# Kernel optimization log

Hardware: AMD Instinct MI355X
Metric: run time of the kernel (lower is better)

Reference implementation:

```python
import jax, jax.numpy as jnp
import numpy as np

N = 100000   # nodes
E = 1250000  # edges per graph
D = 64       # in_feats
H = 64       # hidden_dim
C = 129      # num_classes
EPS = 1e-5


def setup_inputs() -> dict:
    key = jax.random.key(0)
    ks = jax.random.split(key, 32)
    nrm = lambda k, s: jax.random.normal(k, s, jnp.float32) * 0.05
    inp = {
        'node_features': jax.random.normal(ks[0], (N, D), jnp.float32),
        'm_src': jax.random.randint(ks[1], (E,), 0, N, jnp.int32),
        'm_dst': jax.random.randint(ks[2], (E,), 0, N, jnp.int32),
        'r_src': jax.random.randint(ks[3], (E,), 0, N, jnp.int32),
        'r_dst': jax.random.randint(ks[4], (E,), 0, N, jnp.int32),
    }
    i = 5
    for pre in ('soc', 'rt'):
        inp[pre + '_W1'] = nrm(ks[i], (D, H)); inp[pre + '_b1'] = jnp.zeros((H,), jnp.float32)
        inp[pre + '_g1'] = jnp.ones((H,), jnp.float32); inp[pre + '_bt1'] = jnp.zeros((H,), jnp.float32)
        inp[pre + '_W2'] = nrm(ks[i + 1], (H, H)); inp[pre + '_b2'] = jnp.zeros((H,), jnp.float32)
        inp[pre + '_g2'] = jnp.ones((H,), jnp.float32); inp[pre + '_bt2'] = jnp.zeros((H,), jnp.float32)
        i += 2
    inp['gW1'] = nrm(ks[i], (4 * H, H)); inp['gb1'] = jnp.zeros((H,), jnp.float32)
    inp['prelu_a'] = jnp.full((1,), 0.25, jnp.float32)
    inp['gW2'] = nrm(ks[i + 1], (H, H)); inp['gb2'] = jnp.zeros((H,), jnp.float32)
    inp['fcW'] = nrm(ks[i + 2], (H, C)); inp['fcb'] = jnp.zeros((C,), jnp.float32)
    return inp


def _gconv(h, src, dst, W, b):
    # DGL GraphConv, norm='both': D_out^{-1/2} (scatter-sum) D_in^{-1/2}, linear, ELU
    ones = jnp.ones(src.shape[0], jnp.float32)
    deg_o = jax.ops.segment_sum(ones, src, num_segments=N)
    deg_i = jax.ops.segment_sum(ones, dst, num_segments=N)
    ns = jax.lax.rsqrt(jnp.clip(deg_o, 1.0))
    nd = jax.lax.rsqrt(jnp.clip(deg_i, 1.0))
    agg = jax.ops.segment_sum((h * ns[:, None])[src], dst, num_segments=N)
    return jax.nn.elu((agg * nd[:, None]) @ W + b)


def _bn(x, g, b):
    mu = x.mean(0)
    v = x.var(0)
    return (x - mu) * jax.lax.rsqrt(v + EPS) * g + b


def _branch(x, src, dst, W1, b1, g1, bt1, W2, b2, g2, bt2):
    h = _bn(_gconv(x, src, dst, W1, b1), g1, bt1)
    return _bn(_gconv(h, src, dst, W2, b2), g2, bt2)


def reference(node_features, m_src, m_dst, r_src, r_dst,
              soc_W1, soc_b1, soc_g1, soc_bt1, soc_W2, soc_b2, soc_g2, soc_bt2,
              rt_W1, rt_b1, rt_g1, rt_bt1, rt_W2, rt_b2, rt_g2, rt_bt2,
              gW1, gb1, prelu_a, gW2, gb2, fcW, fcb):
    h1 = _branch(node_features, m_src, m_dst, soc_W1, soc_b1, soc_g1, soc_bt1, soc_W2, soc_b2, soc_g2, soc_bt2)
    h2 = _branch(node_features, r_src, r_dst, rt_W1, rt_b1, rt_g1, rt_bt1, rt_W2, rt_b2, rt_g2, rt_bt2)
    cat = jnp.concatenate([h1, h2, jnp.abs(h1 - h2), h1 * h2], axis=-1)
    z = cat @ gW1 + gb1
    z = jnp.where(z > 0, z, prelu_a * z)  # PReLU (single shared slope)
    gate = jax.nn.sigmoid(z @ gW2 + gb2)
    fused = gate * h1 + (1.0 - gate) * h2
    return fused @ fcW + fcb
```

## Files before the change

kernel.cpp:

```cpp
#include <hip/hip_runtime.h>
#include <math.h>

#define NN 100000
#define NE 1250000
#define HD 64
#define NCLS 129
#define NTILES 6250
#define GRID_T 782
#define MAXDEG 64

#define NCH 64
#define CHU ((NE + NCH - 1) / NCH)
#define SUBR 50000
#define NW2 12500
#define NHE2 ((NN + 1) * (size_t)HD)

typedef float f32x4 __attribute__((ext_vector_type(4)));
typedef short bf16x8 __attribute__((ext_vector_type(8)));

__device__ __forceinline__ short f2b(float f) {
    unsigned u = __builtin_bit_cast(unsigned, f);
    u += 0x7FFFu + ((u >> 16) & 1u);
    return (short)(u >> 16);
}
__device__ __forceinline__ float b2f(short s) {
    return __builtin_bit_cast(float, ((unsigned)(unsigned short)s) << 16);
}

__global__ __launch_bounds__(1024) void k_hist8(
    const int* __restrict__ d0, const int* __restrict__ s0,
    const int* __restrict__ d1, const int* __restrict__ s1,
    unsigned char* __restrict__ P8d, unsigned char* __restrict__ P8s) {
    __shared__ unsigned int hw[NW2];
    int b = blockIdx.x, s = blockIdx.y, z = blockIdx.z;
    int g = z >> 1, arr = z & 1;
    const int* __restrict__ idx = arr ? (g ? s1 : s0) : (g ? d1 : d0);
    for (int i = threadIdx.x; i < NW2; i += 1024) hw[i] = 0;
    __syncthreads();
    int lo = s * SUBR;
    int beg = b * CHU, end = beg + CHU;
    if (end > NE) end = NE;
    for (int i = beg + threadIdx.x; i < end; i += 1024) {
        int v = idx[i] - lo;
        if ((unsigned)v < (unsigned)SUBR)
            atomicAdd(&hw[v >> 2], 1u << ((v & 3) * 8));
    }
    __syncthreads();
    unsigned char* base = arr ? P8s : P8d;
    unsigned int* dst = (unsigned int*)(base + ((size_t)(g * NCH + b)) * NN + lo);
    for (int i = threadIdx.x; i < NW2; i += 1024) dst[i] = hw[i];
}

__global__ void k_reduce8(unsigned int* __restrict__ Pd, const unsigned int* __restrict__ Ps,
                          float* __restrict__ ns, float* __restrict__ nd,
                          int* __restrict__ degi) {
    int w = blockIdx.x * 256 + threadIdx.x;
    if (w >= NN / 4) return;
    int g = blockIdx.y;
    Pd += (size_t)g * NCH * (NN / 4);
    Ps += (size_t)g * NCH * (NN / 4);
    ns += (size_t)g * (NN + 1); nd += (size_t)g * NN; degi += (size_t)g * NN;
    if (w == 0) ns[NN] = 0.f;
    unsigned run = 0;
#pragma unroll 8
    for (int b = 0; b < NCH; ++b) {
        size_t o = (size_t)b * (NN / 4) + w;
        unsigned v = Pd[o];
        Pd[o] = run;
        run += v;
    }
    unsigned so = 0;
#pragma unroll 8
    for (int b = 0; b < NCH; ++b) so += Ps[(size_t)b * (NN / 4) + w];
#pragma unroll
    for (int j = 0; j < 4; ++j) {
        int din = (run >> (8 * j)) & 255;
        int dout = (so >> (8 * j)) & 255;
        int node = w * 4 + j;
        degi[node] = din;
        ns[node] = rsqrtf((float)(dout < 1 ? 1 : dout));
        nd[node] = rsqrtf((float)(din < 1 ? 1 : din));
    }
}

__global__ __launch_bounds__(1024) void k_fill8(
    const int* __restrict__ d0, const int* __restrict__ d1,
    const int* __restrict__ s0, const int* __restrict__ s1,
    const unsigned char* __restrict__ Pofs, int* __restrict__ col) {
    __shared__ unsigned int cur[NW2];
    int b = blockIdx.x, s = blockIdx.y, g = blockIdx.z;
    const int* __restrict__ dst = g ? d1 : d0;
    const int* __restrict__ src = g ? s1 : s0;
    col += ((size_t)g * NN) * MAXDEG;
    const unsigned char* __restrict__ ofs = Pofs + ((size_t)(g * NCH + b)) * NN;
    for (int i = threadIdx.x; i < NW2; i += 1024) cur[i] = 0;
    __syncthreads();
    int lo = s * SUBR;
    int beg = b * CHU, end = beg + CHU;
    if (end > NE) end = NE;
    for (int i = beg + threadIdx.x; i < end; i += 1024) {
        int d = dst[i] - lo;
        if ((unsigned)d < (unsigned)SUBR) {
            unsigned old = atomicAdd(&cur[d >> 2], 1u << ((d & 3) * 8));
            int r = (old >> ((d & 3) * 8)) & 255;
            int node = d + lo;
            col[(size_t)node * MAXDEG + (int)ofs[node] + r] = src[i];
        }
    }
}

__global__ void k_scale_nf(const float* __restrict__ nf, short* __restrict__ T) {
    int i = blockIdx.x * blockDim.x + threadIdx.x;
    if (i >= (NN + 1) * 8) return;
    int node = i >> 3;
    short r[8];
    if (node == NN) {
#pragma unroll
        for (int j = 0; j < 8; ++j) r[j] = 0;
    } else {
        const float4* p = (const float4*)(nf + (size_t)i * 8);
        float4 a = p[0], b = p[1];
        r[0] = f2b(a.x); r[1] = f2b(a.y); r[2] = f2b(a.z); r[3] = f2b(a.w);
        r[4] = f2b(b.x); r[5] = f2b(b.y); r[6] = f2b(b.z); r[7] = f2b(b.w);
    }
    *(bf16x8*)(T + (size_t)i * 8) = *(bf16x8*)r;
}

template <int BN>
__global__ __launch_bounds__(256) void k_gather(
    const short* __restrict__ tab, size_t tabStride,
    const float* __restrict__ ns, const float* __restrict__ nd,
    const int* __restrict__ degi, const int* __restrict__ col,
    short* __restrict__ out, const float* __restrict__ stats,
    const float* __restrict__ ga, const float* __restrict__ gb,
    const float* __restrict__ bta, const float* __restrict__ btb) {
    int w = (blockIdx.x * 256 + threadIdx.x) >> 6;
    int lane = threadIdx.x & 63;
    if (w >= NN) return;
    int g = blockIdx.y;
    tab += (size_t)g * tabStride; nd += (size_t)g * NN; degi += (size_t)g * NN;
    col += ((size_t)g * NN) * MAXDEG; out += (size_t)g * NHE2;
    const float* nsA = ns + (size_t)g * (NN + 1);
    int grp = lane >> 4;
    int sub = lane & 15;
    int deg = degi[w];
    int myc = (lane < deg) ? col[(size_t)w * MAXDEG + lane] : NN;
    float myns = nsA[myc];
    float a0 = 0.f, a1 = 0.f, a2 = 0.f, a3 = 0.f, sl = 0.f;
    for (int j = 0; j < deg; j += 16) {
#pragma unroll
        for (int u = 0; u < 4; ++u) {
            int idx = j + u * 4 + grp;
            int c = __shfl(myc, idx, 64);
            float nsc = __shfl(myns, idx, 64);
            uint2 v = *(const uint2*)(tab + (size_t)c * HD + sub * 4);
            a0 = fmaf(nsc, __builtin_bit_cast(float, v.x << 16), a0);
            a1 = fmaf(nsc, __builtin_bit_cast(float, v.x & 0xffff0000u), a1);
            a2 = fmaf(nsc, __builtin_bit_cast(float, v.y << 16), a2);
            a3 = fmaf(nsc, __builtin_bit_cast(float, v.y & 0xffff0000u), a3);
            if (BN) sl += nsc;
        }
    }
    a0 += __shfl_xor(a0, 16, 64); a1 += __shfl_xor(a1, 16, 64);
    a2 += __shfl_xor(a2, 16, 64); a3 += __shfl_xor(a3, 16, 64);
    a0 += __shfl_xor(a0, 32, 64); a1 += __shfl_xor(a1, 32, 64);
    a2 += __shfl_xor(a2, 32, 64); a3 += __shfl_xor(a3, 32, 64);
    if (BN) { sl += __shfl_xor(sl, 16, 64); sl += __shfl_xor(sl, 32, 64); }
    if (grp == 0) {
        float s = nd[w];
        float r4[4] = {a0, a1, a2, a3};
        if (BN) {
            const float* gp = g ? gb : ga;
            const float* bp = g ? btb : bta;
            const float* st = stats + (size_t)g * 128;
            const float invN = 1.f / (float)NN;
#pragma unroll
            for (int q = 0; q < 4; ++q) {
                int o = sub * 4 + q;
                float mu = st[o] * invN;
                float var = fmaxf(st[64 + o] * invN - mu * mu, 0.f);
                float isd = rsqrtf(var + 1e-5f);
                float sc = gp[o] * isd;
                float sh = bp[o] - mu * sc;
                r4[q] = s * (sc * r4[q] + sh * sl);
            }
        } else {
#pragma unroll
            for (int q = 0; q < 4; ++q) r4[q] *= s;
        }
        unsigned r0 = ((unsigned)(unsigned short)f2b(r4[0])) |
                      (((unsigned)(unsigned short)f2b(r4[1])) << 16);
        unsigned r1 = ((unsigned)(unsigned short)f2b(r4[2])) |
                      (((unsigned)(unsigned short)f2b(r4[3])) << 16);
        uint2 r; r.x = r0; r.y = r1;
        *(uint2*)(out + (size_t)w * HD + sub * 4) = r;
    }
}

__global__ __launch_bounds__(256) void k_lin(
    const short* __restrict__ X, const float* __restrict__ Wa, const float* __restrict__ Wb,
    const float* __restrict__ ba, const float* __restrict__ bb,
    short* __restrict__ Y, float* __restrict__ stats) {
    __shared__ short sW[4096];
    __shared__ float sm2[128];
    int g = blockIdx.y;
    const float* W = g ? Wb : Wa;
    const float* bias = g ? bb : ba;
    X += (size_t)g * NHE2; Y += (size_t)g * NHE2; stats += (size_t)g * 128;
    int t = threadIdx.x;
    for (int i = t; i < 4096; i += 256) {
        int j = i & 7, l16i = (i >> 3) & 15, kgi = (i >> 7) & 3, kbi = (i >> 9) & 1, oti = (i >> 10) & 3;
        sW[i] = f2b(W[(kbi * 32 + kgi * 8 + j) * HD + oti * 16 + l16i]);
    }
    if (t < 128) sm2[t] = 0.f;
    __syncthreads();
    int lane = t & 63, wv = t >> 6, l16 = lane & 15, kg = lane >> 4;
    bf16x8 bfrag[2][4];
#pragma unroll
    for (int kb = 0; kb < 2; ++kb)
#pragma unroll
        for (int ot = 0; ot < 4; ++ot)
            bfrag[kb][ot] = *(const bf16x8*)&sW[((ot * 2 + kb) * 4 + kg) * 128 + l16 * 8];
    float bo[4];
#pragma unroll
    for (int ot = 0; ot < 4; ++ot) bo[ot] = bias[ot * 16 + l16];
    float ps[4] = {0.f, 0.f, 0.f, 0.f}, pq[4] = {0.f, 0.f, 0.f, 0.f};
    for (int tile = blockIdx.x * 4 + wv; tile < NTILES; tile += GRID_T * 4) {
        const short* xp = X + ((size_t)tile * 16 + l16) * HD + kg * 8;
        bf16x8 a0 = *(const bf16x8*)xp;
        bf16x8 a1 = *(const bf16x8*)(xp + 32);
        f32x4 acc[4];
#pragma unroll
        for (int ot = 0; ot < 4; ++ot) {
            acc[ot] = (f32x4){0.f, 0.f, 0.f, 0.f};
            acc[ot] = __builtin_amdgcn_mfma_f32_16x16x32_bf16(a0, bfrag[0][ot], acc[ot], 0, 0, 0);
            acc[ot] = __builtin_amdgcn_mfma_f32_16x16x32_bf16(a1, bfrag[1][ot], acc[ot], 0, 0, 0);
        }
#pragma unroll
        for (int ot = 0; ot < 4; ++ot) {
#pragma unroll
            for (int r = 0; r < 4; ++r) {
                float y = acc[ot][r] + bo[ot];
                y = y > 0.f ? y : expm1f(y);
                ps[ot] += y; pq[ot] += y * y;
                Y[((size_t)tile * 16 + kg * 4 + r) * HD + ot * 16 + l16] = f2b(y);
            }
        }
    }
#pragma unroll
    for (int ot = 0; ot < 4; ++ot) {
        atomicAdd(&sm2[ot * 16 + l16], ps[ot]);
        atomicAdd(&sm2[64 + ot * 16 + l16], pq[ot]);
    }
    __syncthreads();
    if (t < 128) atomicAdd(&stats[t], sm2[t]);
}

__global__ void k_bnb(const short* __restrict__ Y, short* __restrict__ O,
                      const float* __restrict__ stats,
                      const float* __restrict__ ga, const float* __restrict__ gb,
                      const float* __restrict__ bta, const float* __restrict__ btb) {
    int i = blockIdx.x * blockDim.x + threadIdx.x;
    if (i >= NN * 8) return;
    int gI = blockIdx.y;
    Y += (size_t)gI * NHE2; O += (size_t)gI * NHE2; stats += (size_t)gI * 128;
    const float* g = gI ? gb : ga;
    const float* bt = gI ? btb : bta;
    int o0 = (i & 7) * 8;
    bf16x8 v = *(const bf16x8*)(Y + (size_t)i * 8);
    short r[8];
    const float invN = 1.f / (float)NN;
#pragma unroll
    for (int j = 0; j < 8; ++j) {
        int o = o0 + j;
        float mu = stats[o] * invN;
        float var = fmaxf(stats[64 + o] * invN - mu * mu, 0.f);
        float isd = rsqrtf(var + 1e-5f);
        float sc = g[o] * isd;
        float sh = bt[o] - mu * sc;
        r[j] = f2b(b2f(v[j]) * sc + sh);
    }
    *(bf16x8*)(O + (size_t)i * 8) = *(bf16x8*)r;
}

#define TRS 72
__global__ __launch_bounds__(256) void k_tail(
    const short* __restrict__ H1, const short* __restrict__ H2,
    const float* __restrict__ W1, const float* __restrict__ bias1,
    const float* __restrict__ pa,
    const float* __restrict__ W2, const float* __restrict__ bias2,
    const float* __restrict__ Wf, const float* __restrict__ biasf,
    float* __restrict__ out) {
    __shared__ short sW1[16384];
    __shared__ short sW2[4096];
    __shared__ short sWf[9216];
    __shared__ short tr[4][2][16 * TRS];
    int t = threadIdx.x;
    for (int i = t; i < 16384; i += 256) {
        int j = i & 7, l16i = (i >> 3) & 15, kgi = (i >> 7) & 3, kbi = (i >> 9) & 7, oti = (i >> 12) & 3;
        sW1[i] = f2b(W1[(kbi * 32 + kgi * 8 + j) * HD + oti * 16 + l16i]);
    }
    for (int i = t; i < 4096; i += 256) {
        int j = i & 7, l16i = (i >> 3) & 15, kgi = (i >> 7) & 3, kbi = (i >> 9) & 1, oti = (i >> 10) & 3;
        sW2[i] = f2b(W2[(kbi * 32 + kgi * 8 + j) * HD + oti * 16 + l16i]);
    }
    for (int i = t; i < 9216; i += 256) {
        int j = i & 7, l16i = (i >> 3) & 15, kgi = (i >> 7) & 3, kbi = (i >> 9) & 1, oti = i >> 10;
        int k = kbi * 32 + kgi * 8 + j, o = oti * 16 + l16i;
        sWf[i] = (o < NCLS) ? f2b(Wf[k * NCLS + o]) : (short)0;
    }
    __syncthreads();
    int lane = t & 63, wv = t >> 6, l16 = lane & 15, kg = lane >> 4;
    float slope = pa[0];
    float bo1[4], bo2[4], bof[9];
#pragma unroll
    for (int ot = 0; ot < 4; ++ot) { bo1[ot] = bias1[ot * 16 + l16]; bo2[ot] = bias2[ot * 16 + l16]; }
#pragma unroll
    for (int ot = 0; ot < 9; ++ot) {
        int o = ot * 16 + l16;
        bof[ot] = (o < NCLS) ? biasf[o] : 0.f;
    }
    bf16x8 b2frag[2][4];
#pragma unroll
    for (int kb = 0; kb < 2; ++kb)
#pragma unroll
        for (int ot = 0; ot < 4; ++ot)
            b2frag[kb][ot] = *(const bf16x8*)&sW2[((ot * 2 + kb) * 4 + kg) * 128 + l16 * 8];
    short* trZ = &tr[wv][0][0];
    short* trG = &tr[wv][1][0];

    for (int tile = blockIdx.x * 4 + wv; tile < NTILES; tile += GRID_T * 4) {
        size_t rb = ((size_t)tile * 16 + l16) * HD + kg * 8;
        bf16x8 h1e = *(const bf16x8*)(H1 + rb);
        bf16x8 h1o = *(const bf16x8*)(H1 + rb + 32);
        bf16x8 h2e = *(const bf16x8*)(H2 + rb);
        bf16x8 h2o = *(const bf16x8*)(H2 + rb + 32);
        bf16x8 fe[8];
        fe[0] = h1e; fe[1] = h1o; fe[2] = h2e; fe[3] = h2o;
        short tabs[8], tprd[8];
#pragma unroll
        for (int j = 0; j < 8; ++j) {
            float a = b2f(h1e[j]), b = b2f(h2e[j]);
            tabs[j] = f2b(fabsf(a - b)); tprd[j] = f2b(a * b);
        }
        fe[4] = *(bf16x8*)tabs; fe[6] = *(bf16x8*)tprd;
#pragma unroll
        for (int j = 0; j < 8; ++j) {
            float a = b2f(h1o[j]), b = b2f(h2o[j]);
            tabs[j] = f2b(fabsf(a - b)); tprd[j] = f2b(a * b);
        }
        fe[5] = *(bf16x8*)tabs; fe[7] = *(bf16x8*)tprd;
        f32x4 acc[4];
#pragma unroll
        for (int ot = 0; ot < 4; ++ot) acc[ot] = (f32x4){0.f, 0.f, 0.f, 0.f};
#pragma unroll
        for (int kb = 0; kb < 8; ++kb)
#pragma unroll
            for (int ot = 0; ot < 4; ++ot) {
                bf16x8 bf = *(const bf16x8*)&sW1[((ot * 8 + kb) * 4 + kg) * 128 + l16 * 8];
                acc[ot] = __builtin_amdgcn_mfma_f32_16x16x32_bf16(fe[kb], bf, acc[ot], 0, 0, 0);
            }
#pragma unroll
        for (int ot = 0; ot < 4; ++ot)
#pragma unroll
            for (int r = 0; r < 4; ++r) {
                float z = acc[ot][r] + bo1[ot];
                z = z > 0.f ? z : slope * z;
                trZ[(kg * 4 + r) * TRS + ot * 16 + l16] = f2b(z);
            }
        asm volatile("s_waitcnt lgkmcnt(0)" ::: "memory");
        __builtin_amdgcn_sched_barrier(0);
        bf16x8 za0 = *(const bf16x8*)&trZ[l16 * TRS + kg * 8];
        bf16x8 za1 = *(const bf16x8*)&trZ[l16 * TRS + 32 + kg * 8];
        f32x4 acc2[4];
#pragma unroll
        for (int ot = 0; ot < 4; ++ot) {
            acc2[ot] = (f32x4){0.f, 0.f, 0.f, 0.f};
            acc2[ot] = __builtin_amdgcn_mfma_f32_16x16x32_bf16(za0, b2frag[0][ot], acc2[ot], 0, 0, 0);
            acc2[ot] = __builtin_amdgcn_mfma_f32_16x16x32_bf16(za1, b2frag[1][ot], acc2[ot], 0, 0, 0);
        }
#pragma unroll
        for (int ot = 0; ot < 4; ++ot)
#pragma unroll
            for (int r = 0; r < 4; ++r) {
                float y = acc2[ot][r] + bo2[ot];
                float gate = 1.f / (1.f + expf(-y));
                trG[(kg * 4 + r) * TRS + ot * 16 + l16] = f2b(gate);
            }
        asm volatile("s_waitcnt lgkmcnt(0)" ::: "memory");
        __builtin_amdgcn_sched_barrier(0);
        bf16x8 ga0 = *(const bf16x8*)&trG[l16 * TRS + kg * 8];
        bf16x8 ga1 = *(const bf16x8*)&trG[l16 * TRS + 32 + kg * 8];
        short f0[8], f1[8];
#pragma unroll
        for (int j = 0; j < 8; ++j) {
            float gf = b2f(ga0[j]);
            f0[j] = f2b(gf * b2f(h1e[j]) + (1.f - gf) * b2f(h2e[j]));
            float gf2 = b2f(ga1[j]);
            f1[j] = f2b(gf2 * b2f(h1o[j]) + (1.f - gf2) * b2f(h2o[j]));
        }
        bf16x8 fa0 = *(bf16x8*)f0, fa1 = *(bf16x8*)f1;
        f32x4 acc3[9];
#pragma unroll
        for (int ot = 0; ot < 9; ++ot) acc3[ot] = (f32x4){0.f, 0.f, 0.f, 0.f};
#pragma unroll
        for (int kb = 0; kb < 2; ++kb) {
            bf16x8 a = kb ? fa1 : fa0;
#pragma unroll
            for (int ot = 0; ot < 9; ++ot) {
                bf16x8 bf = *(const bf16x8*)&sWf[((ot * 2 + kb) * 4 + kg) * 128 + l16 * 8];
                acc3[ot] = __builtin_amdgcn_mfma_f32_16x16x32_bf16(a, bf, acc3[ot], 0, 0, 0);
            }
        }
#pragma unroll
        for (int ot = 0; ot < 9; ++ot) {
            int o = ot * 16 + l16;
            if (o < NCLS) {
#pragma unroll
                for (int r = 0; r < 4; ++r) {
                    int node = tile * 16 + kg * 4 + r;
                    out[(size_t)node * NCLS + o] = acc3[ot][r] + bof[ot];
                }
            }
        }
    }
}

extern "C" void kernel_launch(void* const* d_in, const int* in_sizes, int n_in,
                              void* d_out, int out_size, void* d_ws, size_t ws_size,
                              hipStream_t stream) {
    (void)in_sizes; (void)n_in; (void)out_size; (void)ws_size;
    const int N = NN;

    const float* nf = (const float*)d_in[0];
    const int* m_src = (const int*)d_in[1];
    const int* m_dst = (const int*)d_in[2];
    const int* r_src = (const int*)d_in[3];
    const int* r_dst = (const int*)d_in[4];
    const float *W1[2], *b1[2], *g1[2], *bt1[2], *W2[2], *b2[2], *g2[2], *bt2[2];
    for (int br = 0; br < 2; ++br) {
        int base = 5 + br * 8;
        W1[br] = (const float*)d_in[base + 0];
        b1[br] = (const float*)d_in[base + 1];
        g1[br] = (const float*)d_in[base + 2];
        bt1[br] = (const float*)d_in[base + 3];
        W2[br] = (const float*)d_in[base + 4];
        b2[br] = (const float*)d_in[base + 5];
        g2[br] = (const float*)d_in[base + 6];
        bt2[br] = (const float*)d_in[base + 7];
    }
    const float* gW1 = (const float*)d_in[21];
    const float* gb1 = (const float*)d_in[22];
    const float* pa  = (const float*)d_in[23];
    const float* gW2 = (const float*)d_in[24];
    const float* gb2 = (const float*)d_in[25];
    const float* fcW = (const float*)d_in[26];
    const float* fcb = (const float*)d_in[27];
    float* out = (float*)d_out;

    char* p = (char*)d_ws;
    auto take = [&](size_t bytes) { char* r = p; p += (bytes + 255) & ~(size_t)255; return r; };
    size_t NHb2 = NHE2 * 2;
    unsigned char* P8d = (unsigned char*)take((size_t)2 * NCH * NN);
    unsigned char* P8s = (unsigned char*)take((size_t)2 * NCH * NN);
    int* col  = (int*)take((size_t)2 * NN * MAXDEG * 4);
    short* T  = (short*)take(NHb2);
    short* X  = (short*)take(2 * NHb2);
    short* Y  = (short*)take(2 * NHb2);
    short* H  = (short*)take(2 * NHb2);
    float* ns = (float*)take((size_t)2 * (N + 1) * 4);
    float* nd = (float*)take((size_t)2 * N * 4);
    float* stats = (float*)take(2 * 2 * 128 * 4);
    int* degi = (int*)take((size_t)2 * N * 4);

    int gEWz = ((N + 1) * 8 + 255) / 256;
    int gEW  = (N * 8 + 255) / 256;
    int gW4 = (N / 4 + 255) / 256;
    int gGat = (N * 64) / 256;

    k_hist8<<<dim3(NCH, 2, 4), 1024, 0, stream>>>(m_dst, m_src, r_dst, r_src, P8d, P8s);
    k_reduce8<<<dim3(gW4, 2), 256, 0, stream>>>((unsigned int*)P8d, (const unsigned int*)P8s,
                                                ns, nd, degi);
    k_fill8<<<dim3(NCH, 2, 2), 1024, 0, stream>>>(m_dst, r_dst, m_src, r_src, P8d, col);
    hipMemsetAsync(stats, 0, 2 * 2 * 128 * 4, stream);

    k_scale_nf<<<gEWz, 256, 0, stream>>>(nf, T);
    k_gather<0><<<dim3(gGat, 2), 256, 0, stream>>>(T, 0, ns, nd, degi, col, X,
                                                   nullptr, nullptr, nullptr, nullptr, nullptr);
    k_lin<<<dim3(GRID_T, 2), 256, 0, stream>>>(X, W1[0], W1[1], b1[0], b1[1], Y, stats);

    k_gather<1><<<dim3(gGat, 2), 256, 0, stream>>>(Y, NHE2, ns, nd, degi, col, X,
                                                   stats, g1[0], g1[1], bt1[0], bt1[1]);
    k_lin<<<dim3(GRID_T, 2), 256, 0, stream>>>(X, W2[0], W2[1], b2[0], b2[1], Y, stats + 256);
    k_bnb<<<dim3(gEW, 2), 256, 0, stream>>>(Y, H, stats + 256, g2[0], g2[1], bt2[0], bt2[1]);

    k_tail<<<GRID_T, 256, 0, stream>>>(H, H + NHE2, gW1, gb1, pa, gW2, gb2, fcW, fcb, out);
}
```

Measured before the change: 370.8 us.

## Prescale layer-1 output by source norm and widen gather loads to 16 bytes

The first linear kernel now multiplies its ELU output by the source-degree norm before storing it. The second gather therefore becomes a plain sum without a per-edge shuffle or FMA by ns. The per-node sum of ns, needed to fold in the BN shift, is computed once in the first gather and stored for reuse. The gather also switches from 8-byte to 16-byte row loads, with 8 lanes per row and 8 edges in flight, which cuts the number of shuffle-reduction steps. The cost is an extra buffer, an ns read per row in k_lin, and zeroing the dummy row.

```diff
diff --git a/kernel.cpp b/kernel.cpp
--- a/kernel.cpp
+++ b/kernel.cpp
@@ -126,12 +126,13 @@
     *(bf16x8*)(T + (size_t)i * 8) = *(bf16x8*)r;
 }
 
-template <int BN>
+template <int PHASE>
 __global__ __launch_bounds__(256) void k_gather(
     const short* __restrict__ tab, size_t tabStride,
     const float* __restrict__ ns, const float* __restrict__ nd,
     const int* __restrict__ degi, const int* __restrict__ col,
-    short* __restrict__ out, const float* __restrict__ stats,
+    short* __restrict__ out, float* __restrict__ sns,
+    const float* __restrict__ stats,
     const float* __restrict__ ga, const float* __restrict__ gb,
     const float* __restrict__ bta, const float* __restrict__ btb) {
     int w = (blockIdx.x * 256 + threadIdx.x) >> 6;
@@ -139,74 +140,92 @@
     if (w >= NN) return;
     int g = blockIdx.y;
     tab += (size_t)g * tabStride; nd += (size_t)g * NN; degi += (size_t)g * NN;
-    col += ((size_t)g * NN) * MAXDEG; out += (size_t)g * NHE2;
+    col += ((size_t)g * NN) * MAXDEG; out += (size_t)g * NHE2; sns += (size_t)g * NN;
     const float* nsA = ns + (size_t)g * (NN + 1);
-    int grp = lane >> 4;
-    int sub = lane & 15;
+    int grp = lane >> 3;
+    int sub = lane & 7;
     int deg = degi[w];
     int myc = (lane < deg) ? col[(size_t)w * MAXDEG + lane] : NN;
-    float myns = nsA[myc];
-    float a0 = 0.f, a1 = 0.f, a2 = 0.f, a3 = 0.f, sl = 0.f;
-    for (int j = 0; j < deg; j += 16) {
+    float myns = 0.f;
+    if (PHASE == 0) myns = nsA[myc];
+    float a[8] = {0.f, 0.f, 0.f, 0.f, 0.f, 0.f, 0.f, 0.f};
+    float sl = 0.f;
+    for (int j = 0; j < deg; j += 32) {
 #pragma unroll
         for (int u = 0; u < 4; ++u) {
-            int idx = j + u * 4 + grp;
+            int idx = j + u * 8 + grp;
             int c = __shfl(myc, idx, 64);
-            float nsc = __shfl(myns, idx, 64);
-            uint2 v = *(const uint2*)(tab + (size_t)c * HD + sub * 4);
-            a0 = fmaf(nsc, __builtin_bit_cast(float, v.x << 16), a0);
-            a1 = fmaf(nsc, __builtin_bit_cast(float, v.x & 0xffff0000u), a1);
-            a2 = fmaf(nsc, __builtin_bit_cast(float, v.y << 16), a2);
-            a3 = fmaf(nsc, __builtin_bit_cast(float, v.y & 0xffff0000u), a3);
-            if (BN) sl += nsc;
-        }
-    }
-    a0 += __shfl_xor(a0, 16, 64); a1 += __shfl_xor(a1, 16, 64);
-    a2 += __shfl_xor(a2, 16, 64); a3 += __shfl_xor(a3, 16, 64);
-    a0 += __shfl_xor(a0, 32, 64); a1 += __shfl_xor(a1, 32, 64);
-    a2 += __shfl_xor(a2, 32, 64); a3 += __shfl_xor(a3, 32, 64);
-    if (BN) { sl += __shfl_xor(sl, 16, 64); sl += __shfl_xor(sl, 32, 64); }
+            uint4 v = *(const uint4*)(tab + (size_t)c * HD + sub * 8);
+            unsigned wd[4] = {v.x, v.y, v.z, v.w};
+            if (PHASE == 0) {
+                float nsc = __shfl(myns, idx, 64);
+                sl += nsc;
+#pragma unroll
+                for (int q = 0; q < 4; ++q) {
+                    a[2 * q]     = fmaf(nsc, __builtin_bit_cast(float, wd[q] << 16), a[2 * q]);
+                    a[2 * q + 1] = fmaf(nsc, __builtin_bit_cast(float, wd[q] & 0xffff0000u), a[2 * q + 1]);
+                }
+            } else {
+#pragma unroll
+                for (int q = 0; q < 4; ++q) {
+                    a[2 * q]     += __builtin_bit_cast(float, wd[q] << 16);
+                    a[2 * q + 1] += __builtin_bit_cast(float, wd[q] & 0xffff0000u);
+                }
+            }
+        }
+    }
+#pragma unroll
+    for (int m = 8; m <= 32; m <<= 1) {
+#pragma unroll
+        for (int q = 0; q < 8; ++q) a[q] += __shfl_xor(a[q], m, 64);
+        if (PHASE == 0) sl += __shfl_xor(sl, m, 64);
+    }
     if (grp == 0) {
         float s = nd[w];
-        float r4[4] = {a0, a1, a2, a3};
-        if (BN) {
+        float r8[8];
+        if (PHASE == 1) {
             const float* gp = g ? gb : ga;
             const float* bp = g ? btb : bta;
             const float* st = stats + (size_t)g * 128;
+            float slv = sns[w];
             const float invN = 1.f / (float)NN;
 #pragma unroll
-            for (int q = 0; q < 4; ++q) {
-                int o = sub * 4 + q;
+            for (int q = 0; q < 8; ++q) {
+                int o = sub * 8 + q;
                 float mu = st[o] * invN;
                 float var = fmaxf(st[64 + o] * invN - mu * mu, 0.f);
                 float isd = rsqrtf(var + 1e-5f);
                 float sc = gp[o] * isd;
                 float sh = bp[o] - mu * sc;
-                r4[q] = s * (sc * r4[q] + sh * sl);
+                r8[q] = s * (sc * a[q] + sh * slv);
             }
         } else {
 #pragma unroll
-            for (int q = 0; q < 4; ++q) r4[q] *= s;
-        }
-        unsigned r0 = ((unsigned)(unsigned short)f2b(r4[0])) |
-                      (((unsigned)(unsigned short)f2b(r4[1])) << 16);
-        unsigned r1 = ((unsigned)(unsigned short)f2b(r4[2])) |
-                      (((unsigned)(unsigned short)f2b(r4[3])) << 16);
-        uint2 r; r.x = r0; r.y = r1;
-        *(uint2*)(out + (size_t)w * HD + sub * 4) = r;
-    }
-}
-
+            for (int q = 0; q < 8; ++q) r8[q] = a[q] * s;
+        }
+        unsigned ow[4];
+#pragma unroll
+        for (int q = 0; q < 4; ++q)
+            ow[q] = ((unsigned)(unsigned short)f2b(r8[2 * q])) |
+                    (((unsigned)(unsigned short)f2b(r8[2 * q + 1])) << 16);
+        uint4 stv; stv.x = ow[0]; stv.y = ow[1]; stv.z = ow[2]; stv.w = ow[3];
+        *(uint4*)(out + (size_t)w * HD + sub * 8) = stv;
+        if (PHASE == 0 && lane == 0) sns[w] = sl;
+    }
+}
+
+template <int SO>
 __global__ __launch_bounds__(256) void k_lin(
     const short* __restrict__ X, const float* __restrict__ Wa, const float* __restrict__ Wb,
     const float* __restrict__ ba, const float* __restrict__ bb,
-    short* __restrict__ Y, float* __restrict__ stats) {
+    short* __restrict__ Y, float* __restrict__ stats, const float* __restrict__ ns) {
     __shared__ short sW[4096];
     __shared__ float sm2[128];
     int g = blockIdx.y;
     const float* W = g ? Wb : Wa;
     const float* bias = g ? bb : ba;
     X += (size_t)g * NHE2; Y += (size_t)g * NHE2; stats += (size_t)g * 128;
+    const float* nsA = ns + (size_t)g * (NN + 1);
     int t = threadIdx.x;
     for (int i = t; i < 4096; i += 256) {
         int j = i & 7, l16i = (i >> 3) & 15, kgi = (i >> 7) & 3, kbi = (i >> 9) & 1, oti = (i >> 10) & 3;
@@ -236,6 +255,11 @@
             acc[ot] = __builtin_amdgcn_mfma_f32_16x16x32_bf16(a0, bfrag[0][ot], acc[ot], 0, 0, 0);
             acc[ot] = __builtin_amdgcn_mfma_f32_16x16x32_bf16(a1, bfrag[1][ot], acc[ot], 0, 0, 0);
         }
+        float nsr[4];
+        if (SO) {
+#pragma unroll
+            for (int r = 0; r < 4; ++r) nsr[r] = nsA[tile * 16 + kg * 4 + r];
+        }
 #pragma unroll
         for (int ot = 0; ot < 4; ++ot) {
 #pragma unroll
@@ -243,7 +267,8 @@
                 float y = acc[ot][r] + bo[ot];
                 y = y > 0.f ? y : expm1f(y);
                 ps[ot] += y; pq[ot] += y * y;
-                Y[((size_t)tile * 16 + kg * 4 + r) * HD + ot * 16 + l16] = f2b(y);
+                float outv = SO ? y * nsr[r] : y;
+                Y[((size_t)tile * 16 + kg * 4 + r) * HD + ot * 16 + l16] = f2b(outv);
             }
         }
     }
@@ -254,6 +279,10 @@
     }
     __syncthreads();
     if (t < 128) atomicAdd(&stats[t], sm2[t]);
+    if (SO && blockIdx.x == 0 && t < 16) {
+        uint2 z; z.x = 0; z.y = 0;
+        ((uint2*)(Y + (size_t)NN * HD))[t] = z;
+    }
 }
 
 __global__ void k_bnb(const short* __restrict__ Y, short* __restrict__ O,
@@ -470,6 +499,7 @@
     short* H  = (short*)take(2 * NHb2);
     float* ns = (float*)take((size_t)2 * (N + 1) * 4);
     float* nd = (float*)take((size_t)2 * N * 4);
+    float* sns = (float*)take((size_t)2 * N * 4);
     float* stats = (float*)take(2 * 2 * 128 * 4);
     int* degi = (int*)take((size_t)2 * N * 4);
 
@@ -485,13 +515,13 @@
     hipMemsetAsync(stats, 0, 2 * 2 * 128 * 4, stream);
 
     k_scale_nf<<<gEWz, 256, 0, stream>>>(nf, T);
-    k_gather<0><<<dim3(gGat, 2), 256, 0, stream>>>(T, 0, ns, nd, degi, col, X,
+    k_gather<0><<<dim3(gGat, 2), 256, 0, stream>>>(T, 0, ns, nd, degi, col, X, sns,
                                                    nullptr, nullptr, nullptr, nullptr, nullptr);
-    k_lin<<<dim3(GRID_T, 2), 256, 0, stream>>>(X, W1[0], W1[1], b1[0], b1[1], Y, stats);
-
-    k_gather<1><<<dim3(gGat, 2), 256, 0, stream>>>(Y, NHE2, ns, nd, degi, col, X,
+    k_lin<1><<<dim3(GRID_T, 2), 256, 0, stream>>>(X, W1[0], W1[1], b1[0], b1[1], Y, stats, ns);
+
+    k_gather<1><<<dim3(gGat, 2), 256, 0, stream>>>(Y, NHE2, ns, nd, degi, col, X, sns,
                                                    stats, g1[0], g1[1], bt1[0], bt1[1]);
-    k_lin<<<dim3(GRID_T, 2), 256, 0, stream>>>(X, W2[0], W2[1], b2[0], b2[1], Y, stats + 256);
+    k_lin<0><<<dim3(GRID_T, 2), 256, 0, stream>>>(X, W2[0], W2[1], b2[0], b2[1], Y, stats + 256, ns);
     k_bnb<<<dim3(gEW, 2), 256, 0, stream>>>(Y, H, stats + 256, g2[0], g2[1], bt2[0], bt2[1]);
 
     k_tail<<<GRID_T, 256, 0, stream>>>(H, H + NHE2, gW1, gb1, pa, gW2, gb2, fcW, fcb, out);
```

Result: slower. 401.4 us (+8.2%).

## Pre-scale source rows by out-degree norm before gather, drop per-edge norm lookups

Applied to the files above, without the earlier changes.

The source-side normalization ns is now folded into the producer kernels (k_scale_nf writes a per-graph ns-scaled bf16 table; the first k_lin multiplies its ELU output by ns). The gather then sums raw neighbour rows without a dependent per-edge load and multiply of ns. The neighbour sum of ns needed for the BN shift is computed once in phase 0 and stored for phase 1. This doubles the initial table size and rounds scaled values to bf16 earlier, which can change numerics slightly.

```diff
diff --git a/kernel.cpp b/kernel.cpp
--- a/kernel.cpp
+++ b/kernel.cpp
@@ -109,70 +109,76 @@
     }
 }
 
-__global__ void k_scale_nf(const float* __restrict__ nf, short* __restrict__ T) {
+__global__ void k_scale_nf(const float* __restrict__ nf, const float* __restrict__ ns,
+                           short* __restrict__ T) {
     int i = blockIdx.x * blockDim.x + threadIdx.x;
     if (i >= (NN + 1) * 8) return;
+    int g = blockIdx.y;
+    ns += (size_t)g * (NN + 1); T += (size_t)g * NHE2;
     int node = i >> 3;
     short r[8];
     if (node == NN) {
 #pragma unroll
         for (int j = 0; j < 8; ++j) r[j] = 0;
     } else {
+        float s = ns[node];
         const float4* p = (const float4*)(nf + (size_t)i * 8);
         float4 a = p[0], b = p[1];
-        r[0] = f2b(a.x); r[1] = f2b(a.y); r[2] = f2b(a.z); r[3] = f2b(a.w);
-        r[4] = f2b(b.x); r[5] = f2b(b.y); r[6] = f2b(b.z); r[7] = f2b(b.w);
+        r[0] = f2b(a.x * s); r[1] = f2b(a.y * s); r[2] = f2b(a.z * s); r[3] = f2b(a.w * s);
+        r[4] = f2b(b.x * s); r[5] = f2b(b.y * s); r[6] = f2b(b.z * s); r[7] = f2b(b.w * s);
     }
     *(bf16x8*)(T + (size_t)i * 8) = *(bf16x8*)r;
 }
 
-template <int BN>
+template <int PHASE>
 __global__ __launch_bounds__(256) void k_gather(
-    const short* __restrict__ tab, size_t tabStride,
-    const float* __restrict__ ns, const float* __restrict__ nd,
-    const int* __restrict__ degi, const int* __restrict__ col,
-    short* __restrict__ out, const float* __restrict__ stats,
+    const short* __restrict__ tab, const float* __restrict__ ns,
+    const float* __restrict__ nd, const int* __restrict__ degi,
+    const int* __restrict__ col, short* __restrict__ out, float* __restrict__ sns,
+    const float* __restrict__ stats,
     const float* __restrict__ ga, const float* __restrict__ gb,
     const float* __restrict__ bta, const float* __restrict__ btb) {
     int w = (blockIdx.x * 256 + threadIdx.x) >> 6;
     int lane = threadIdx.x & 63;
     if (w >= NN) return;
     int g = blockIdx.y;
-    tab += (size_t)g * tabStride; nd += (size_t)g * NN; degi += (size_t)g * NN;
-    col += ((size_t)g * NN) * MAXDEG; out += (size_t)g * NHE2;
+    tab += (size_t)g * NHE2; nd += (size_t)g * NN; degi += (size_t)g * NN;
+    col += ((size_t)g * NN) * MAXDEG; out += (size_t)g * NHE2; sns += (size_t)g * NN;
     const float* nsA = ns + (size_t)g * (NN + 1);
     int grp = lane >> 4;
     int sub = lane & 15;
     int deg = degi[w];
     int myc = (lane < deg) ? col[(size_t)w * MAXDEG + lane] : NN;
-    float myns = nsA[myc];
-    float a0 = 0.f, a1 = 0.f, a2 = 0.f, a3 = 0.f, sl = 0.f;
+    float a0 = 0.f, a1 = 0.f, a2 = 0.f, a3 = 0.f;
     for (int j = 0; j < deg; j += 16) {
 #pragma unroll
         for (int u = 0; u < 4; ++u) {
-            int idx = j + u * 4 + grp;
-            int c = __shfl(myc, idx, 64);
-            float nsc = __shfl(myns, idx, 64);
+            int c = __shfl(myc, j + u * 4 + grp, 64);
             uint2 v = *(const uint2*)(tab + (size_t)c * HD + sub * 4);
-            a0 = fmaf(nsc, __builtin_bit_cast(float, v.x << 16), a0);
-            a1 = fmaf(nsc, __builtin_bit_cast(float, v.x & 0xffff0000u), a1);
-            a2 = fmaf(nsc, __builtin_bit_cast(float, v.y << 16), a2);
-            a3 = fmaf(nsc, __builtin_bit_cast(float, v.y & 0xffff0000u), a3);
-            if (BN) sl += nsc;
+            a0 += __builtin_bit_cast(float, v.x << 16);
+            a1 += __builtin_bit_cast(float, v.x & 0xffff0000u);
+            a2 += __builtin_bit_cast(float, v.y << 16);
+            a3 += __builtin_bit_cast(float, v.y & 0xffff0000u);
         }
     }
     a0 += __shfl_xor(a0, 16, 64); a1 += __shfl_xor(a1, 16, 64);
     a2 += __shfl_xor(a2, 16, 64); a3 += __shfl_xor(a3, 16, 64);
     a0 += __shfl_xor(a0, 32, 64); a1 += __shfl_xor(a1, 32, 64);
     a2 += __shfl_xor(a2, 32, 64); a3 += __shfl_xor(a3, 32, 64);
-    if (BN) { sl += __shfl_xor(sl, 16, 64); sl += __shfl_xor(sl, 32, 64); }
+    if (PHASE == 0) {
+        float sl = nsA[myc];
+#pragma unroll
+        for (int m = 1; m <= 32; m <<= 1) sl += __shfl_xor(sl, m, 64);
+        if (lane == 0) sns[w] = sl;
+    }
     if (grp == 0) {
         float s = nd[w];
         float r4[4] = {a0, a1, a2, a3};
-        if (BN) {
+        if (PHASE == 1) {
             const float* gp = g ? gb : ga;
             const float* bp = g ? btb : bta;
             const float* st = stats + (size_t)g * 128;
+            float slv = sns[w];
             const float invN = 1.f / (float)NN;
 #pragma unroll
             for (int q = 0; q < 4; ++q) {
@@ -182,7 +188,7 @@
                 float isd = rsqrtf(var + 1e-5f);
                 float sc = gp[o] * isd;
                 float sh = bp[o] - mu * sc;
-                r4[q] = s * (sc * r4[q] + sh * sl);
+                r4[q] = s * (sc * r4[q] + sh * slv);
             }
         } else {
 #pragma unroll
@@ -197,16 +203,18 @@
     }
 }
 
+template <int SO>
 __global__ __launch_bounds__(256) void k_lin(
     const short* __restrict__ X, const float* __restrict__ Wa, const float* __restrict__ Wb,
     const float* __restrict__ ba, const float* __restrict__ bb,
-    short* __restrict__ Y, float* __restrict__ stats) {
+    short* __restrict__ Y, float* __restrict__ stats, const float* __restrict__ ns) {
     __shared__ short sW[4096];
     __shared__ float sm2[128];
     int g = blockIdx.y;
     const float* W = g ? Wb : Wa;
     const float* bias = g ? bb : ba;
     X += (size_t)g * NHE2; Y += (size_t)g * NHE2; stats += (size_t)g * 128;
+    const float* nsA = ns + (size_t)g * (NN + 1);
     int t = threadIdx.x;
     for (int i = t; i < 4096; i += 256) {
         int j = i & 7, l16i = (i >> 3) & 15, kgi = (i >> 7) & 3, kbi = (i >> 9) & 1, oti = (i >> 10) & 3;
@@ -236,6 +244,11 @@
             acc[ot] = __builtin_amdgcn_mfma_f32_16x16x32_bf16(a0, bfrag[0][ot], acc[ot], 0, 0, 0);
             acc[ot] = __builtin_amdgcn_mfma_f32_16x16x32_bf16(a1, bfrag[1][ot], acc[ot], 0, 0, 0);
         }
+        float nsr[4];
+        if (SO) {
+#pragma unroll
+            for (int r = 0; r < 4; ++r) nsr[r] = nsA[tile * 16 + kg * 4 + r];
+        }
 #pragma unroll
         for (int ot = 0; ot < 4; ++ot) {
 #pragma unroll
@@ -243,7 +256,8 @@
                 float y = acc[ot][r] + bo[ot];
                 y = y > 0.f ? y : expm1f(y);
                 ps[ot] += y; pq[ot] += y * y;
-                Y[((size_t)tile * 16 + kg * 4 + r) * HD + ot * 16 + l16] = f2b(y);
+                float outv = SO ? y * nsr[r] : y;
+                Y[((size_t)tile * 16 + kg * 4 + r) * HD + ot * 16 + l16] = f2b(outv);
             }
         }
     }
@@ -254,6 +268,10 @@
     }
     __syncthreads();
     if (t < 128) atomicAdd(&stats[t], sm2[t]);
+    if (SO && blockIdx.x == 0 && t < 16) {
+        uint2 z; z.x = 0; z.y = 0;
+        ((uint2*)(Y + (size_t)NN * HD))[t] = z;
+    }
 }
 
 __global__ void k_bnb(const short* __restrict__ Y, short* __restrict__ O,
@@ -464,12 +482,13 @@
     unsigned char* P8d = (unsigned char*)take((size_t)2 * NCH * NN);
     unsigned char* P8s = (unsigned char*)take((size_t)2 * NCH * NN);
     int* col  = (int*)take((size_t)2 * NN * MAXDEG * 4);
-    short* T  = (short*)take(NHb2);
+    short* T  = (short*)take(2 * NHb2);
     short* X  = (short*)take(2 * NHb2);
     short* Y  = (short*)take(2 * NHb2);
     short* H  = (short*)take(2 * NHb2);
     float* ns = (float*)take((size_t)2 * (N + 1) * 4);
     float* nd = (float*)take((size_t)2 * N * 4);
+    float* sns = (float*)take((size_t)2 * N * 4);
     float* stats = (float*)take(2 * 2 * 128 * 4);
     int* degi = (int*)take((size_t)2 * N * 4);
 
@@ -484,14 +503,14 @@
     k_fill8<<<dim3(NCH, 2, 2), 1024, 0, stream>>>(m_dst, r_dst, m_src, r_src, P8d, col);
     hipMemsetAsync(stats, 0, 2 * 2 * 128 * 4, stream);
 
-    k_scale_nf<<<gEWz, 256, 0, stream>>>(nf, T);
-    k_gather<0><<<dim3(gGat, 2), 256, 0, stream>>>(T, 0, ns, nd, degi, col, X,
+    k_scale_nf<<<dim3(gEWz, 2), 256, 0, stream>>>(nf, ns, T);
+    k_gather<0><<<dim3(gGat, 2), 256, 0, stream>>>(T, ns, nd, degi, col, X, sns,
                                                    nullptr, nullptr, nullptr, nullptr, nullptr);
-    k_lin<<<dim3(GRID_T, 2), 256, 0, stream>>>(X, W1[0], W1[1], b1[0], b1[1], Y, stats);
-
-    k_gather<1><<<dim3(gGat, 2), 256, 0, stream>>>(Y, NHE2, ns, nd, degi, col, X,
+    k_lin<1><<<dim3(GRID_T, 2), 256, 0, stream>>>(X, W1[0], W1[1], b1[0], b1[1], Y, stats, ns);
+
+    k_gather<1><<<dim3(gGat, 2), 256, 0, stream>>>(Y, ns, nd, degi, col, X, sns,
                                                    stats, g1[0], g1[1], bt1[0], bt1[1]);
-    k_lin<<<dim3(GRID_T, 2), 256, 0, stream>>>(X, W2[0], W2[1], b2[0], b2[1], Y, stats + 256);
+    k_lin<0><<<dim3(GRID_T, 2), 256, 0, stream>>>(X, W2[0], W2[1], b2[0], b2[1], Y, stats + 256, ns);
     k_bnb<<<dim3(gEW, 2), 256, 0, stream>>>(Y, H, stats + 256, g2[0], g2[1], bt2[0], bt2[1]);
 
     k_tail<<<GRID_T, 256, 0, stream>>>(H, H + NHE2, gW1, gb1, pa, gW2, gb2, fcW, fcb, out);
```

Measured after the change: 387.3 us. 4.4% more time.
